# Performance work log

Measured on AMD Instinct MI355X. Metric: run time of the kernel, lower is better.

The kernel has to match this reference:

```python
import jax, jax.numpy as jnp
import numpy as np

POOL = 4      # pool_size
SR = 2        # sampling_ratio (fixed; torchvision adaptive default approximated)
C_IN = 1024
C1, C2 = 256, 128
OUT_DIM = 2048


def setup_inputs() -> dict:
    key = jax.random.key(0)
    ks = jax.random.split(key, 10)
    B, C, H, W = 8, C_IN, 64, 64
    N = 64
    x = jax.random.normal(ks[0], (B, C, H, W), dtype=jnp.float32)
    # boxes in image pixel coords (image is H*16 = 1024 px)
    img = 1024.0
    x1 = jax.random.uniform(ks[1], (B, N), minval=0.0, maxval=img - 260.0)
    y1 = jax.random.uniform(ks[2], (B, N), minval=0.0, maxval=img - 260.0)
    bw = jax.random.uniform(ks[3], (B, N), minval=32.0, maxval=256.0)
    bh = jax.random.uniform(ks[4], (B, N), minval=32.0, maxval=256.0)
    boxes = jnp.stack([x1, y1, x1 + bw, y1 + bh], axis=-1)  # [B,N,4]
    scale = jnp.float32(1.0 / 16.0)
    # detector params
    w1 = jax.random.normal(ks[5], (C1, C_IN), dtype=jnp.float32) / np.sqrt(C_IN)
    b1 = jnp.zeros((C1,), dtype=jnp.float32)
    w2 = jax.random.normal(ks[6], (C2, C1), dtype=jnp.float32) / np.sqrt(C1)
    b2 = jnp.zeros((C2,), dtype=jnp.float32)
    wl = jax.random.normal(ks[7], (OUT_DIM, C2 * POOL * POOL), dtype=jnp.float32) / np.sqrt(C2 * POOL * POOL)
    bl = jnp.zeros((OUT_DIM,), dtype=jnp.float32)
    return {"x": x, "boxes": boxes, "scale": scale,
            "w1": w1, "b1": b1, "w2": w2, "b2": b2, "wl": wl, "bl": bl}


def _axis_coords(start, size, H):
    # start,size: [R]; returns coords [R, POOL*SR], valid mask, int low/high, lerp wts
    bin_sz = size / POOL                       # [R]
    j = jnp.arange(POOL * SR, dtype=jnp.float32)
    off = jnp.floor(j / SR) + ((j % SR) + 0.5) / SR   # [P]
    c = start[:, None] + off[None, :] * bin_sz[:, None]  # [R,P]
    valid = (c >= -1.0) & (c <= H)
    c = jnp.clip(c, 0.0, H - 1.0)
    lo = jnp.floor(c).astype(jnp.int32)
    lo = jnp.minimum(lo, H - 1)
    hi = jnp.minimum(lo + 1, H - 1)
    frac = c - lo.astype(c.dtype)
    return valid, lo, hi, frac


def _roi_align(feat, boxes, scale):
    # feat: [B,C,H,W], boxes: [B,N,4] -> pooled [B*N, C, POOL, POOL]
    B, C, H, W = feat.shape
    N = boxes.shape[1]
    R = B * N
    bx = (boxes.reshape(R, 4) * scale)
    x1, y1, x2, y2 = bx[:, 0], bx[:, 1], bx[:, 2], bx[:, 3]
    rw = jnp.maximum(x2 - x1, 1.0)
    rh = jnp.maximum(y2 - y1, 1.0)
    vy, y_lo, y_hi, ly = _axis_coords(y1, rh, H)   # [R,P]
    vx, x_lo, x_hi, lx = _axis_coords(x1, rw, W)
    hy, hx = 1.0 - ly, 1.0 - lx
    bidx = jnp.repeat(jnp.arange(B, dtype=jnp.int32), N)  # [R]
    b = bidx[:, None, None]
    # gather 4 corners -> [R,P,P,C]
    v00 = feat[b, :, y_lo[:, :, None], x_lo[:, None, :]]
    v01 = feat[b, :, y_lo[:, :, None], x_hi[:, None, :]]
    v10 = feat[b, :, y_hi[:, :, None], x_lo[:, None, :]]
    v11 = feat[b, :, y_hi[:, :, None], x_hi[:, None, :]]
    w00 = (hy[:, :, None] * hx[:, None, :])[..., None]
    w01 = (hy[:, :, None] * lx[:, None, :])[..., None]
    w10 = (ly[:, :, None] * hx[:, None, :])[..., None]
    w11 = (ly[:, :, None] * lx[:, None, :])[..., None]
    val = v00 * w00 + v01 * w01 + v10 * w10 + v11 * w11
    mask = (vy[:, :, None] & vx[:, None, :])[..., None]
    val = jnp.where(mask, val, 0.0)            # [R,P,P,C]
    val = val.reshape(R, POOL, SR, POOL, SR, C).mean(axis=(2, 4))  # [R,POOL,POOL,C]
    return jnp.transpose(val, (0, 3, 1, 2))    # [R,C,POOL,POOL]


def reference(x, boxes, scale, w1, b1, w2, b2, wl, bl):
    pooled = _roi_align(x, boxes, scale)                  # [R,C,4,4]
    h = jax.nn.elu(jnp.einsum('rchw,oc->rohw', pooled, w1) + b1[None, :, None, None])
    h = jax.nn.elu(jnp.einsum('rchw,oc->rohw', h, w2) + b2[None, :, None, None])
    h = h.reshape(h.shape[0], -1)                         # [R, 128*16], torch Flatten order
    out = jax.nn.elu(h @ wl.T + bl)                       # [R, 2048]
    return out
```

## Files before the change

### kernel.cpp

```cpp
#include <hip/hip_runtime.h>
#include <math.h>

#define C_INK   1024
#define C1D     256
#define C2D     128
#define OUTD    2048
#define R_ROI   512
#define MPIX    32768

typedef _Float16 half8 __attribute__((ext_vector_type(8)));
typedef float    f32x4 __attribute__((ext_vector_type(4)));

__device__ __forceinline__ unsigned int pack2h(float a, float b) {
    union { _Float16 h[2]; unsigned int u; } p;
    p.h[0] = (_Float16)a; p.h[1] = (_Float16)b;
    return p.u;
}
__device__ __forceinline__ float eluf(float v) { return v > 0.f ? v : expf(v) - 1.f; }

template<int RC>
__device__ __forceinline__ half8* ldsq(_Float16* base, int row, int ch) {
    return reinterpret_cast<half8*>(base) + row * RC + (ch ^ (row & 7));
}

__global__ __launch_bounds__(256) void cvt_weights(
    const float* __restrict__ s1, _Float16* __restrict__ d1, int n1,
    const float* __restrict__ s2, _Float16* __restrict__ d2, int n2,
    const float* __restrict__ s3, _Float16* __restrict__ d3, int n3)
{
    int i = (blockIdx.x * 256 + threadIdx.x) * 4;
    const float* s; _Float16* d;
    if (i < n1)            { s = s1; d = d1; }
    else if (i < n1 + n2)  { s = s2; d = d2; i -= n1; }
    else                   { s = s3; d = d3; i -= n1 + n2; if (i >= n3) return; }
    const float4 v = *reinterpret_cast<const float4*>(s + i);
    uint2 u; u.x = pack2h(v.x, v.y); u.y = pack2h(v.z, v.w);
    *reinterpret_cast<uint2*>(d + i) = u;
}

__global__ __launch_bounds__(512, 4) void conv1x1_f16(
    const float* __restrict__ x, const _Float16* __restrict__ w1h,
    _Float16* __restrict__ z)
{
    __shared__ __align__(16) _Float16 As[64 * 64];
    __shared__ __align__(16) _Float16 Bs[256 * 64];

    const int tid  = threadIdx.x;
    const int lane = tid & 63;
    const int wave = tid >> 6;
    const int m0   = blockIdx.x * 64;
    const int b    = m0 >> 12;
    const int p0   = m0 & 4095;

    const int bc  = tid & 7;
    const int br0 = tid >> 3;

    float ar[8];
    half8 brg[4];
    f32x4 acc[4][2];
    #pragma unroll
    for (int i = 0; i < 4; ++i)
        #pragma unroll
        for (int j = 0; j < 2; ++j) acc[i][j] = (f32x4){0.f, 0.f, 0.f, 0.f};

    const float* xbase = x + (size_t)b * C_INK * 4096 + p0 + lane;

    auto LOADT = [&](int k0) {
        const float* xk = xbase + (size_t)(k0 + wave * 8) * 4096;
        #pragma unroll
        for (int j = 0; j < 8; ++j) ar[j] = xk[(size_t)j * 4096];
        #pragma unroll
        for (int i = 0; i < 4; ++i)
            brg[i] = *reinterpret_cast<const half8*>(
                &w1h[(size_t)(br0 + i * 64) * C_INK + k0 + bc * 8]);
    };
    auto WRITET = [&]() {
        union { half8 h; unsigned int u[4]; } pk;
        #pragma unroll
        for (int j = 0; j < 4; ++j) pk.u[j] = pack2h(ar[2 * j], ar[2 * j + 1]);
        *ldsq<8>(As, lane, wave) = pk.h;
        #pragma unroll
        for (int i = 0; i < 4; ++i) *ldsq<8>(Bs, br0 + i * 64, bc) = brg[i];
    };
    auto COMPUTET = [&]() {
        #pragma unroll
        for (int kk = 0; kk < 2; ++kk) {
            const int ch = kk * 4 + (lane >> 4);
            half8 af[4], bf[2];
            #pragma unroll
            for (int mi = 0; mi < 4; ++mi) af[mi] = *ldsq<8>(As, mi * 16 + (lane & 15), ch);
            #pragma unroll
            for (int ni = 0; ni < 2; ++ni) bf[ni] = *ldsq<8>(Bs, wave * 32 + ni * 16 + (lane & 15), ch);
            #pragma unroll
            for (int mi = 0; mi < 4; ++mi)
                #pragma unroll
                for (int ni = 0; ni < 2; ++ni)
                    acc[mi][ni] = __builtin_amdgcn_mfma_f32_16x16x32_f16(bf[ni], af[mi], acc[mi][ni], 0, 0, 0);
        }
    };

    LOADT(0); WRITET(); __syncthreads();
    for (int t = 0; t < 15; ++t) {
        LOADT((t + 1) * 64);
        COMPUTET();
        __syncthreads();
        WRITET();
        __syncthreads();
    }
    COMPUTET();

    _Float16* zp = z + (size_t)m0 * C1D;
    #pragma unroll
    for (int mi = 0; mi < 4; ++mi) {
        const int pixel = mi * 16 + (lane & 15);
        #pragma unroll
        for (int ni = 0; ni < 2; ++ni) {
            const int oc0 = wave * 32 + ni * 16 + (lane >> 4) * 4;
            uint2 u;
            u.x = pack2h(acc[mi][ni][0], acc[mi][ni][1]);
            u.y = pack2h(acc[mi][ni][2], acc[mi][ni][3]);
            *reinterpret_cast<uint2*>(&zp[(size_t)pixel * C1D + oc0]) = u;
        }
    }
}

__global__ __launch_bounds__(512) void roi_gemm2_f16(
    const _Float16* __restrict__ z, const float* __restrict__ boxes,
    const float* __restrict__ scale_p, const float* __restrict__ b1v,
    const _Float16* __restrict__ w2h, const float* __restrict__ b2v,
    _Float16* __restrict__ h2)
{
    __shared__ __align__(16) _Float16 H1s[16 * 256];
    __shared__ int   s_off[64][4];
    __shared__ float s_w[64][4];

    const int bid  = blockIdx.x;
    const int r    = (bid & 7) * 64 + (bid >> 3);
    const int tid  = threadIdx.x;
    const int lane = tid & 63;
    const int wv   = tid >> 6;

    half8 bfr[8];
    {
        const _Float16* wp = w2h + (size_t)(wv * 16 + (lane & 15)) * C1D + (lane >> 4) * 8;
        #pragma unroll
        for (int ks = 0; ks < 8; ++ks)
            bfr[ks] = *reinterpret_cast<const half8*>(wp + ks * 32);
    }

    if (tid < 64) {
        const float sc = scale_p[0];
        const float x1 = boxes[r * 4 + 0] * sc, y1 = boxes[r * 4 + 1] * sc;
        const float x2 = boxes[r * 4 + 2] * sc, y2 = boxes[r * 4 + 3] * sc;
        const float rw = fmaxf(x2 - x1, 1.f), rh = fmaxf(y2 - y1, 1.f);
        const int jy = tid >> 3, jx = tid & 7;

        float offy = (float)(jy >> 1) + (float)(jy & 1) * 0.5f + 0.25f;
        float cy = y1 + offy * rh * 0.25f;
        const bool vy = (cy >= -1.f) && (cy <= 64.f);
        cy = fminf(fmaxf(cy, 0.f), 63.f);
        int ylo = (int)cy; if (ylo > 63) ylo = 63;
        int yhi = ylo + 1; if (yhi > 63) yhi = 63;
        const float ly = cy - (float)ylo, hy = 1.f - ly;

        float offx = (float)(jx >> 1) + (float)(jx & 1) * 0.5f + 0.25f;
        float cx = x1 + offx * rw * 0.25f;
        const bool vx = (cx >= -1.f) && (cx <= 64.f);
        cx = fminf(fmaxf(cx, 0.f), 63.f);
        int xlo = (int)cx; if (xlo > 63) xlo = 63;
        int xhi = xlo + 1; if (xhi > 63) xhi = 63;
        const float lx = cx - (float)xlo, hx = 1.f - lx;

        const float wm = (vy && vx) ? 0.25f : 0.f;
        s_w[tid][0] = hy * hx * wm;
        s_w[tid][1] = hy * lx * wm;
        s_w[tid][2] = ly * hx * wm;
        s_w[tid][3] = ly * lx * wm;
        s_off[tid][0] = (ylo * 64 + xlo) * C1D;
        s_off[tid][1] = (ylo * 64 + xhi) * C1D;
        s_off[tid][2] = (yhi * 64 + xlo) * C1D;
        s_off[tid][3] = (yhi * 64 + xhi) * C1D;
    }
    __syncthreads();

    {
        const int ch8  = tid & 31;
        const int cell = tid >> 5;
        const _Float16* zb = z + (size_t)(r >> 6) * 4096 * C1D + ch8 * 8;

        float accv[8];
        #pragma unroll
        for (int e = 0; e < 8; ++e) accv[e] = 0.f;

        const int py = cell >> 2, px = cell & 3;
        #pragma unroll
        for (int u = 0; u < 4; ++u) {
            const int s = (py * 2 + (u >> 1)) * 8 + px * 2 + (u & 1);
            #pragma unroll
            for (int k = 0; k < 4; ++k) {
                const half8 v = *reinterpret_cast<const half8*>(zb + s_off[s][k]);
                const float w = s_w[s][k];
                #pragma unroll
                for (int e = 0; e < 8; ++e) accv[e] += (float)v[e] * w;
            }
        }

        const float4 b0 = *reinterpret_cast<const float4*>(&b1v[ch8 * 8]);
        const float4 b4 = *reinterpret_cast<const float4*>(&b1v[ch8 * 8 + 4]);
        half8 o;
        o[0] = (_Float16)eluf(accv[0] + b0.x); o[1] = (_Float16)eluf(accv[1] + b0.y);
        o[2] = (_Float16)eluf(accv[2] + b0.z); o[3] = (_Float16)eluf(accv[3] + b0.w);
        o[4] = (_Float16)eluf(accv[4] + b4.x); o[5] = (_Float16)eluf(accv[5] + b4.y);
        o[6] = (_Float16)eluf(accv[6] + b4.z); o[7] = (_Float16)eluf(accv[7] + b4.w);
        *ldsq<32>(H1s, cell, ch8) = o;
    }
    __syncthreads();

    f32x4 oa = (f32x4){0.f, 0.f, 0.f, 0.f};
    #pragma unroll
    for (int ks = 0; ks < 8; ++ks) {
        const int ch = ks * 4 + (lane >> 4);
        const half8 af = *ldsq<32>(H1s, lane & 15, ch);
        oa = __builtin_amdgcn_mfma_f32_16x16x32_f16(af, bfr[ks], oa, 0, 0, 0);
    }

    {
        const int o  = wv * 16 + (lane & 15);
        const int p0 = (lane >> 4) * 4;
        const float bv = b2v[o];
        uint2 u;
        u.x = pack2h(eluf(oa[0] + bv), eluf(oa[1] + bv));
        u.y = pack2h(eluf(oa[2] + bv), eluf(oa[3] + bv));
        *reinterpret_cast<uint2*>(&h2[(size_t)r * 2048 + o * 16 + p0]) = u;
    }
}

__global__ __launch_bounds__(512) void gemm_nt_out(
    const _Float16* __restrict__ A, const _Float16* __restrict__ W,
    const float* __restrict__ bias, float* __restrict__ Cout)
{
    constexpr int K = OUTD, N = OUTD;
    __shared__ __align__(16) _Float16 As[64 * 64];
    __shared__ __align__(16) _Float16 Bs[128 * 64];

    const int bid  = blockIdx.x;
    const int xcd  = bid & 7;
    const int idx  = bid >> 3;
    const int n0   = (xcd * 2 + (idx & 1)) * 128;
    const int m0   = (idx >> 1) * 64;

    const int tid  = threadIdx.x;
    const int lane = tid & 63;
    const int wave = tid >> 6;
    const int wr   = wave >> 2, wc = wave & 3;
    const int c    = tid & 7;
    const int r0   = tid >> 3;

    half8 arg, brg[2];
    f32x4 acc[2][2];
    #pragma unroll
    for (int i = 0; i < 2; ++i)
        #pragma unroll
        for (int j = 0; j < 2; ++j) acc[i][j] = (f32x4){0.f, 0.f, 0.f, 0.f};

    auto LOADT = [&](int k0) {
        arg = *reinterpret_cast<const half8*>(&A[(size_t)(m0 + r0) * K + k0 + c * 8]);
        #pragma unroll
        for (int i = 0; i < 2; ++i)
            brg[i] = *reinterpret_cast<const half8*>(&W[(size_t)(n0 + r0 + i * 64) * K + k0 + c * 8]);
    };
    auto WRITET = [&]() {
        *ldsq<8>(As, r0, c) = arg;
        #pragma unroll
        for (int i = 0; i < 2; ++i) *ldsq<8>(Bs, r0 + i * 64, c) = brg[i];
    };
    auto COMPUTET = [&]() {
        #pragma unroll
        for (int kk = 0; kk < 2; ++kk) {
            const int ch = kk * 4 + (lane >> 4);
            half8 af[2], bf[2];
            #pragma unroll
            for (int mi = 0; mi < 2; ++mi) af[mi] = *ldsq<8>(As, wr * 32 + mi * 16 + (lane & 15), ch);
            #pragma unroll
            for (int ni = 0; ni < 2; ++ni) bf[ni] = *ldsq<8>(Bs, wc * 32 + ni * 16 + (lane & 15), ch);
            #pragma unroll
            for (int mi = 0; mi < 2; ++mi)
                #pragma unroll
                for (int ni = 0; ni < 2; ++ni)
                    acc[mi][ni] = __builtin_amdgcn_mfma_f32_16x16x32_f16(bf[ni], af[mi], acc[mi][ni], 0, 0, 0);
        }
    };

    constexpr int nt = K / 64;
    LOADT(0); WRITET(); __syncthreads();
    for (int t = 0; t < nt - 1; ++t) {
        LOADT((t + 1) * 64);
        COMPUTET();
        __syncthreads();
        WRITET();
        __syncthreads();
    }
    COMPUTET();

    #pragma unroll
    for (int mi = 0; mi < 2; ++mi) {
        const int row = m0 + wr * 32 + mi * 16 + (lane & 15);
        #pragma unroll
        for (int ni = 0; ni < 2; ++ni) {
            const int col0 = n0 + wc * 32 + ni * 16 + (lane >> 4) * 4;
            const float4 bv = *reinterpret_cast<const float4*>(&bias[col0]);
            float4 o;
            o.x = eluf(acc[mi][ni][0] + bv.x);
            o.y = eluf(acc[mi][ni][1] + bv.y);
            o.z = eluf(acc[mi][ni][2] + bv.z);
            o.w = eluf(acc[mi][ni][3] + bv.w);
            *reinterpret_cast<float4*>(&Cout[(size_t)row * N + col0]) = o;
        }
    }
}

extern "C" void kernel_launch(void* const* d_in, const int* in_sizes, int n_in,
                              void* d_out, int out_size, void* d_ws, size_t ws_size,
                              hipStream_t stream) {
    const float* x     = (const float*)d_in[0];
    const float* boxes = (const float*)d_in[1];
    const float* scale = (const float*)d_in[2];
    const float* w1    = (const float*)d_in[3];
    const float* b1    = (const float*)d_in[4];
    const float* w2    = (const float*)d_in[5];
    const float* b2    = (const float*)d_in[6];
    const float* wl    = (const float*)d_in[7];
    const float* bl    = (const float*)d_in[8];
    float* out = (float*)d_out;

    _Float16* z   = (_Float16*)d_ws;
    _Float16* h2  = z   + (size_t)MPIX * C1D;
    _Float16* w1h = h2  + (size_t)R_ROI * OUTD;
    _Float16* w2h = w1h + (size_t)C1D * C_INK;
    _Float16* wlh = w2h + (size_t)C2D * C1D;

    const int n1 = C1D * C_INK, n2 = C2D * C1D, n3 = OUTD * OUTD;

    cvt_weights<<<dim3((n1 + n2 + n3) / 1024), dim3(256), 0, stream>>>(
        w1, w1h, n1, w2, w2h, n2, wl, wlh, n3);

    conv1x1_f16<<<dim3(MPIX / 64), dim3(512), 0, stream>>>(x, w1h, z);

    roi_gemm2_f16<<<dim3(R_ROI), dim3(512), 0, stream>>>(
        z, boxes, scale, b1, w2h, b2, h2);

    gemm_nt_out<<<dim3(128), dim3(512), 0, stream>>>(h2, wlh, bl, out);
}
```

Before: 77.65 us.

## Fold weight conversion into conv kernel and retile output GEMM to 64x64

```diff
diff --git a/kernel.cpp b/kernel.cpp
--- a/kernel.cpp
+++ b/kernel.cpp
@@ -8,6 +8,8 @@
 #define R_ROI   512
 #define MPIX    32768
 
+#define NSIDE   128
+
 typedef _Float16 half8 __attribute__((ext_vector_type(8)));
 typedef float    f32x4 __attribute__((ext_vector_type(4)));
 
@@ -23,32 +25,35 @@
     return reinterpret_cast<half8*>(base) + row * RC + (ch ^ (row & 7));
 }
 
-__global__ __launch_bounds__(256) void cvt_weights(
-    const float* __restrict__ s1, _Float16* __restrict__ d1, int n1,
-    const float* __restrict__ s2, _Float16* __restrict__ d2, int n2,
-    const float* __restrict__ s3, _Float16* __restrict__ d3, int n3)
-{
-    int i = (blockIdx.x * 256 + threadIdx.x) * 4;
-    const float* s; _Float16* d;
-    if (i < n1)            { s = s1; d = d1; }
-    else if (i < n1 + n2)  { s = s2; d = d2; i -= n1; }
-    else                   { s = s3; d = d3; i -= n1 + n2; if (i >= n3) return; }
-    const float4 v = *reinterpret_cast<const float4*>(s + i);
-    uint2 u; u.x = pack2h(v.x, v.y); u.y = pack2h(v.z, v.w);
-    *reinterpret_cast<uint2*>(d + i) = u;
-}
-
 __global__ __launch_bounds__(512, 4) void conv1x1_f16(
-    const float* __restrict__ x, const _Float16* __restrict__ w1h,
+    const float* __restrict__ x, const float* __restrict__ w1,
+    const float* __restrict__ w2, const float* __restrict__ wl,
+    _Float16* __restrict__ w2h, _Float16* __restrict__ wlh,
     _Float16* __restrict__ z)
 {
+    const int bid = blockIdx.x;
+    const int tid = threadIdx.x;
+
+    if (bid < NSIDE) {
+        constexpr int NF4_W2 = (C2D * C1D) / 4;
+        constexpr int NF4    = NF4_W2 + (OUTD * OUTD) / 4;
+        for (int i = bid * 512 + tid; i < NF4; i += NSIDE * 512) {
+            const float* s; _Float16* d; int e;
+            if (i < NF4_W2) { s = w2; d = w2h; e = i * 4; }
+            else            { s = wl; d = wlh; e = (i - NF4_W2) * 4; }
+            const float4 v = *reinterpret_cast<const float4*>(s + e);
+            uint2 u; u.x = pack2h(v.x, v.y); u.y = pack2h(v.z, v.w);
+            *reinterpret_cast<uint2*>(d + e) = u;
+        }
+        return;
+    }
+
     __shared__ __align__(16) _Float16 As[64 * 64];
     __shared__ __align__(16) _Float16 Bs[256 * 64];
 
-    const int tid  = threadIdx.x;
     const int lane = tid & 63;
     const int wave = tid >> 6;
-    const int m0   = blockIdx.x * 64;
+    const int m0   = (bid - NSIDE) * 64;
     const int b    = m0 >> 12;
     const int p0   = m0 & 4095;
 
@@ -70,9 +75,15 @@
         #pragma unroll
         for (int j = 0; j < 8; ++j) ar[j] = xk[(size_t)j * 4096];
         #pragma unroll
-        for (int i = 0; i < 4; ++i)
-            brg[i] = *reinterpret_cast<const half8*>(
-                &w1h[(size_t)(br0 + i * 64) * C_INK + k0 + bc * 8]);
+        for (int i = 0; i < 4; ++i) {
+            const float* wp = &w1[(size_t)(br0 + i * 64) * C_INK + k0 + bc * 8];
+            const float4 v0 = *reinterpret_cast<const float4*>(wp);
+            const float4 v1 = *reinterpret_cast<const float4*>(wp + 4);
+            union { half8 h; unsigned int u[4]; } pk;
+            pk.u[0] = pack2h(v0.x, v0.y); pk.u[1] = pack2h(v0.z, v0.w);
+            pk.u[2] = pack2h(v1.x, v1.y); pk.u[3] = pack2h(v1.z, v1.w);
+            brg[i] = pk.h;
+        }
     };
     auto WRITET = [&]() {
         union { half8 h; unsigned int u[4]; } pk;
@@ -240,14 +251,12 @@
     const float* __restrict__ bias, float* __restrict__ Cout)
 {
     constexpr int K = OUTD, N = OUTD;
-    __shared__ __align__(16) _Float16 As[64 * 64];
-    __shared__ __align__(16) _Float16 Bs[128 * 64];
+    __shared__ __align__(16) _Float16 As[64 * 128];
+    __shared__ __align__(16) _Float16 Bs[64 * 128];
 
     const int bid  = blockIdx.x;
-    const int xcd  = bid & 7;
-    const int idx  = bid >> 3;
-    const int n0   = (xcd * 2 + (idx & 1)) * 128;
-    const int m0   = (idx >> 1) * 64;
+    const int m0   = (bid >> 5) * 64;
+    const int n0   = (bid & 31) * 64;
 
     const int tid  = threadIdx.x;
     const int lane = tid & 63;
@@ -256,45 +265,42 @@
     const int c    = tid & 7;
     const int r0   = tid >> 3;
 
-    half8 arg, brg[2];
-    f32x4 acc[2][2];
-    #pragma unroll
-    for (int i = 0; i < 2; ++i)
-        #pragma unroll
-        for (int j = 0; j < 2; ++j) acc[i][j] = (f32x4){0.f, 0.f, 0.f, 0.f};
+    half8 arg[2], brg[2];
+    f32x4 acc[2];
+    acc[0] = (f32x4){0.f, 0.f, 0.f, 0.f};
+    acc[1] = (f32x4){0.f, 0.f, 0.f, 0.f};
 
     auto LOADT = [&](int k0) {
-        arg = *reinterpret_cast<const half8*>(&A[(size_t)(m0 + r0) * K + k0 + c * 8]);
-        #pragma unroll
-        for (int i = 0; i < 2; ++i)
-            brg[i] = *reinterpret_cast<const half8*>(&W[(size_t)(n0 + r0 + i * 64) * K + k0 + c * 8]);
+        const _Float16* ap = &A[(size_t)(m0 + r0) * K + k0 + c * 16];
+        arg[0] = *reinterpret_cast<const half8*>(ap);
+        arg[1] = *reinterpret_cast<const half8*>(ap + 8);
+        const _Float16* wp = &W[(size_t)(n0 + r0) * K + k0 + c * 16];
+        brg[0] = *reinterpret_cast<const half8*>(wp);
+        brg[1] = *reinterpret_cast<const half8*>(wp + 8);
     };
     auto WRITET = [&]() {
-        *ldsq<8>(As, r0, c) = arg;
-        #pragma unroll
-        for (int i = 0; i < 2; ++i) *ldsq<8>(Bs, r0 + i * 64, c) = brg[i];
+        *ldsq<16>(As, r0, 2 * c)     = arg[0];
+        *ldsq<16>(As, r0, 2 * c + 1) = arg[1];
+        *ldsq<16>(Bs, r0, 2 * c)     = brg[0];
+        *ldsq<16>(Bs, r0, 2 * c + 1) = brg[1];
     };
     auto COMPUTET = [&]() {
         #pragma unroll
-        for (int kk = 0; kk < 2; ++kk) {
+        for (int kk = 0; kk < 4; ++kk) {
             const int ch = kk * 4 + (lane >> 4);
-            half8 af[2], bf[2];
-            #pragma unroll
-            for (int mi = 0; mi < 2; ++mi) af[mi] = *ldsq<8>(As, wr * 32 + mi * 16 + (lane & 15), ch);
-            #pragma unroll
-            for (int ni = 0; ni < 2; ++ni) bf[ni] = *ldsq<8>(Bs, wc * 32 + ni * 16 + (lane & 15), ch);
-            #pragma unroll
-            for (int mi = 0; mi < 2; ++mi)
-                #pragma unroll
-                for (int ni = 0; ni < 2; ++ni)
-                    acc[mi][ni] = __builtin_amdgcn_mfma_f32_16x16x32_f16(bf[ni], af[mi], acc[mi][ni], 0, 0, 0);
-        }
-    };
-
-    constexpr int nt = K / 64;
+            half8 af[2], bf;
+            af[0] = *ldsq<16>(As, wr * 32 + (lane & 15), ch);
+            af[1] = *ldsq<16>(As, wr * 32 + 16 + (lane & 15), ch);
+            bf    = *ldsq<16>(Bs, wc * 16 + (lane & 15), ch);
+            acc[0] = __builtin_amdgcn_mfma_f32_16x16x32_f16(bf, af[0], acc[0], 0, 0, 0);
+            acc[1] = __builtin_amdgcn_mfma_f32_16x16x32_f16(bf, af[1], acc[1], 0, 0, 0);
+        }
+    };
+
+    constexpr int nt = K / 128;
     LOADT(0); WRITET(); __syncthreads();
     for (int t = 0; t < nt - 1; ++t) {
-        LOADT((t + 1) * 64);
+        LOADT((t + 1) * 128);
         COMPUTET();
         __syncthreads();
         WRITET();
@@ -304,18 +310,15 @@
 
     #pragma unroll
     for (int mi = 0; mi < 2; ++mi) {
-        const int row = m0 + wr * 32 + mi * 16 + (lane & 15);
-        #pragma unroll
-        for (int ni = 0; ni < 2; ++ni) {
-            const int col0 = n0 + wc * 32 + ni * 16 + (lane >> 4) * 4;
-            const float4 bv = *reinterpret_cast<const float4*>(&bias[col0]);
-            float4 o;
-            o.x = eluf(acc[mi][ni][0] + bv.x);
-            o.y = eluf(acc[mi][ni][1] + bv.y);
-            o.z = eluf(acc[mi][ni][2] + bv.z);
-            o.w = eluf(acc[mi][ni][3] + bv.w);
-            *reinterpret_cast<float4*>(&Cout[(size_t)row * N + col0]) = o;
-        }
+        const int row  = m0 + wr * 32 + mi * 16 + (lane & 15);
+        const int col0 = n0 + wc * 16 + (lane >> 4) * 4;
+        const float4 bv = *reinterpret_cast<const float4*>(&bias[col0]);
+        float4 o;
+        o.x = eluf(acc[mi][0] + bv.x);
+        o.y = eluf(acc[mi][1] + bv.y);
+        o.z = eluf(acc[mi][2] + bv.z);
+        o.w = eluf(acc[mi][3] + bv.w);
+        *reinterpret_cast<float4*>(&Cout[(size_t)row * N + col0]) = o;
     }
 }
 
@@ -335,19 +338,14 @@
 
     _Float16* z   = (_Float16*)d_ws;
     _Float16* h2  = z   + (size_t)MPIX * C1D;
-    _Float16* w1h = h2  + (size_t)R_ROI * OUTD;
-    _Float16* w2h = w1h + (size_t)C1D * C_INK;
+    _Float16* w2h = h2  + (size_t)R_ROI * OUTD;
     _Float16* wlh = w2h + (size_t)C2D * C1D;
 
-    const int n1 = C1D * C_INK, n2 = C2D * C1D, n3 = OUTD * OUTD;
-
-    cvt_weights<<<dim3((n1 + n2 + n3) / 1024), dim3(256), 0, stream>>>(
-        w1, w1h, n1, w2, w2h, n2, wl, wlh, n3);
-
-    conv1x1_f16<<<dim3(MPIX / 64), dim3(512), 0, stream>>>(x, w1h, z);
+    conv1x1_f16<<<dim3(NSIDE + MPIX / 64), dim3(512), 0, stream>>>(
+        x, w1, w2, wl, w2h, wlh, z);
 
     roi_gemm2_f16<<<dim3(R_ROI), dim3(512), 0, stream>>>(
         z, boxes, scale, b1, w2h, b2, h2);
 
-    gemm_nt_out<<<dim3(128), dim3(512), 0, stream>>>(h2, wlh, bl, out);
-}
+    gemm_nt_out<<<dim3(256), dim3(512), 0, stream>>>(h2, wlh, bl, out);
+}
```

New measurement: 77.90 us. Within noise of the previous version (+0.3%).
